# Kernel optimization log

Measured on AMD Instinct MI355X. Metric: run time of the kernel, lower is better.

Reference implementation:

```python
import jax, jax.numpy as jnp
import numpy as np

D_IN = 512
D = 1024      # new_embed_dim
H = 16        # num_heads
HD = D // H   # head_dim


def setup_inputs() -> dict:
    key = jax.random.key(0)
    ks = jax.random.split(key, 16)
    g = lambda k, shape, fan: jax.random.normal(k, shape, jnp.float32) / np.sqrt(fan)
    return {
        "x1": jax.random.normal(ks[0], (16, 1, D_IN), jnp.float32),
        "x2": jax.random.normal(ks[1], (16, 4096, D_IN), jnp.float32),
        "x3": jax.random.normal(ks[2], (16, 4096, D_IN), jnp.float32),
        # embedding1 (for x1) and embedding2 (used for BOTH x2 and x3, per source)
        "We1": g(ks[3], (D_IN, D), D_IN), "be1": jnp.zeros((D,), jnp.float32),
        "We2": g(ks[4], (D_IN, D), D_IN), "be2": jnp.zeros((D,), jnp.float32),
        "Wq": g(ks[5], (D, D), D), "bq": jnp.zeros((D,), jnp.float32),
        "Wk": g(ks[6], (D, D), D), "bk": jnp.zeros((D,), jnp.float32),
        "Wv": g(ks[7], (D, D), D), "bv": jnp.zeros((D,), jnp.float32),
        "Wo": g(ks[8], (D, D), D), "bo": jnp.zeros((D,), jnp.float32),
    }


def reference(x1, x2, x3, We1, be1, We2, be2, Wq, bq, Wk, bk, Wv, bv, Wo, bo):
    B = x1.shape[0]
    # embeddings (x3 intentionally uses embedding2's weights, matching source)
    x1e = x1 @ We1 + be1                      # [B,1,D]
    x2e = x2 @ We2 + be2                      # [B,S,D]
    x3e = x3 @ We2 + be2                      # [B,S,D]
    q = (x1e @ Wq + bq).reshape(B, -1, H, HD).transpose(0, 2, 1, 3)  # [B,H,1,HD]
    k = (x2e @ Wk + bk).reshape(B, -1, H, HD).transpose(0, 2, 1, 3)  # [B,H,S,HD]
    v = (x3e @ Wv + bv).reshape(B, -1, H, HD).transpose(0, 2, 1, 3)  # [B,H,S,HD]
    scale = jnp.asarray(np.sqrt(HD), q.dtype)
    attn = jax.nn.softmax(jnp.einsum("bhqd,bhkd->bhqk", q, k) / scale, axis=-1)
    # dropout is identity at inference (keras training=False default)
    av = jnp.einsum("bhqk,bhkd->bhqd", attn, v)          # [B,H,1,HD]
    av = av.transpose(0, 2, 1, 3).reshape(B, -1, D)      # [B,1,D]
    out = av @ Wo + bo                                   # [B,1,D]
    return jnp.squeeze(out, axis=1)                      # [B,D]
```

## Files before the change

kernel.cpp:

```cpp
#include <hip/hip_runtime.h>


#define DIN 512
#define DD  1024
#define NH  16
#define HD  64
#define BB  16
#define SS  4096
#define NCH 32

__device__ __forceinline__ int wave_id() {
    return __builtin_amdgcn_readfirstlane((int)(threadIdx.x >> 6));
}

__device__ __forceinline__ void tile_transpose(const float* __restrict__ in,
                                               float* __restrict__ out,
                                               int R, int C, int rblk, int cblk) {
    __shared__ float tl[32][33];
    const int tx = threadIdx.x & 31, ty = threadIdx.x >> 5;
    const int c0 = cblk * 32, r0 = rblk * 32;
#pragma unroll
    for (int k = 0; k < 4; ++k)
        tl[ty + k * 8][tx] = in[(size_t)(r0 + ty + k * 8) * C + c0 + tx];
    __syncthreads();
#pragma unroll
    for (int k = 0; k < 4; ++k)
        out[(size_t)(c0 + ty + k * 8) * R + r0 + tx] = tl[tx][ty + k * 8];
}

__global__ __launch_bounds__(256) void k_prep(const float* __restrict__ We2,
                                              const float* __restrict__ Wk,
                                              const float* __restrict__ be1,
                                              const float* __restrict__ bq,
                                              const float* __restrict__ bv,
                                              const float* __restrict__ bo,
                                              float* __restrict__ We2t,
                                              float* __restrict__ WkT,
                                              float* __restrict__ x1e,
                                              float* __restrict__ qb,
                                              float* __restrict__ av,
                                              float* __restrict__ out) {
    const int bx = blockIdx.x;
    if (bx < 512) {
        tile_transpose(We2, We2t, DIN, DD, bx >> 5, bx & 31);
    } else if (bx < 1536) {
        const int lb = bx - 512;
        tile_transpose(Wk, WkT, DD, DD, lb >> 5, lb & 31);
    } else {
        const int b = bx - 1536;
#pragma unroll
        for (int k = 0; k < 4; ++k) {
            const int c = k * 256 + threadIdx.x;
            x1e[(size_t)b * DD + c] = be1[c];
            qb[(size_t)b * DD + c]  = bq[c];
            av[(size_t)b * DD + c]  = bv[c];
            out[(size_t)b * DD + c] = bo[c];
        }
    }
}

template <int K, int N, int KS, bool HASB>
__global__ __launch_bounds__(256) void k_bmv2(const float* __restrict__ in,
                                              const float* __restrict__ W,
                                              const float* __restrict__ bias,
                                              float* __restrict__ out) {
    const int l = threadIdx.x & 63;
    const int c = blockIdx.x * 64 + l;
    const int wv = wave_id();
    constexpr int KCH = K / KS;
    constexpr int SUB = KCH / 4;
    const float* inb = in + (size_t)blockIdx.y * 16 * K;
    float acc[16];
#pragma unroll
    for (int r = 0; r < 16; ++r) acc[r] = 0.f;
    const int i0 = blockIdx.z * KCH + wv * SUB;
#pragma unroll 4
    for (int i = i0; i < i0 + SUB; ++i) {
        const float wval = W[(size_t)i * N + c];
#pragma unroll
        for (int r = 0; r < 16; ++r) acc[r] += inb[(size_t)r * K + i] * wval;
    }
    __shared__ float red[4][16][64];
#pragma unroll
    for (int r = 0; r < 16; ++r) red[wv][r][l] = acc[r];
    __syncthreads();
#pragma unroll
    for (int k = 0; k < 4; ++k) {
        const int r = wv + k * 4;
        float v = red[0][r][l] + red[1][r][l] + red[2][r][l] + red[3][r][l];
        float* dst = out + ((size_t)blockIdx.y * 16 + r) * N + c;
        if (KS == 1) {
            if (HASB) v += bias[c];
            *dst = v;
        } else {
            atomicAdd(dst, v);
        }
    }
}

__global__ __launch_bounds__(256) void k_u2(const float* __restrict__ q,
                                            const float* __restrict__ WkT,
                                            float* __restrict__ u) {
    const int h = blockIdx.y;
    const int l = threadIdx.x & 63;
    const int c = blockIdx.x * 64 + l;
    const int wv = wave_id();
    float acc[16];
#pragma unroll
    for (int bb = 0; bb < 16; ++bb) acc[bb] = 0.f;
#pragma unroll 4
    for (int dk = 0; dk < 16; ++dk) {
        const int d = wv * 16 + dk;
        const float wval = WkT[(size_t)(h * HD + d) * DD + c];
#pragma unroll
        for (int bb = 0; bb < 16; ++bb)
            acc[bb] += q[(size_t)bb * DD + h * HD + d] * wval;
    }
    __shared__ float red[4][16][64];
#pragma unroll
    for (int bb = 0; bb < 16; ++bb) red[wv][bb][l] = acc[bb];
    __syncthreads();
#pragma unroll
    for (int k = 0; k < 4; ++k) {
        const int bb = wv + k * 4;
        float v = red[0][bb][l] + red[1][bb][l] + red[2][bb][l] + red[3][bb][l];
        u[((size_t)bb * NH + h) * DD + c] = v;
    }
}

__global__ __launch_bounds__(256) void k_attn(const float* __restrict__ x2,
                                              const float* __restrict__ x3,
                                              const float* __restrict__ w,
                                              float* __restrict__ gp,
                                              float* __restrict__ mls) {
    __shared__ __align__(16) char smem[64 * 33 * 16 + 16 * 64 * 4];
    float4* tile = (float4*)smem;
    float*  scb  = (float*)(smem + 64 * 33 * 16);
    float*  red  = (float*)smem;
    __shared__ float sm[4][16], sl[4][16];

    const int b = blockIdx.y, ch = blockIdx.x;
    const int l = threadIdx.x & 63;
    const int wv = wave_id();
    const int h0 = wv * 4;
    const float4* wp = (const float4*)(w + ((size_t)b * NH + h0) * DIN);

    float m[16], lsum[16], acc[16][8];
#pragma unroll
    for (int h = 0; h < 16; ++h) {
        m[h] = -1e30f; lsum[h] = 0.f;
#pragma unroll
        for (int j = 0; j < 8; ++j) acc[h][j] = 0.f;
    }

    for (int t = 0; t < 2; ++t) {
        const int s0 = ch * 128 + t * 64;
        const float4* x2f = (const float4*)x2 + ((size_t)b * SS + s0) * (DIN / 4);
        float a0 = 0.f, a1 = 0.f, a2 = 0.f, a3 = 0.f;
        for (int kt = 0; kt < 4; ++kt) {
            __syncthreads();
#pragma unroll
            for (int k = 0; k < 8; ++k) {
                const int idx = threadIdx.x + k * 256;
                const int row = idx >> 5, c4 = idx & 31;
                tile[row * 33 + c4] = x2f[row * (DIN / 4) + kt * 32 + c4];
            }
            __syncthreads();
#pragma unroll 8
            for (int c4 = 0; c4 < 32; ++c4) {
                const float4 x = tile[l * 33 + c4];
                const float4 q0 = wp[kt * 32 + c4];
                const float4 q1 = wp[128 + kt * 32 + c4];
                const float4 q2 = wp[256 + kt * 32 + c4];
                const float4 q3 = wp[384 + kt * 32 + c4];
                a0 += x.x * q0.x + x.y * q0.y + x.z * q0.z + x.w * q0.w;
                a1 += x.x * q1.x + x.y * q1.y + x.z * q1.z + x.w * q1.w;
                a2 += x.x * q2.x + x.y * q2.y + x.z * q2.z + x.w * q2.w;
                a3 += x.x * q3.x + x.y * q3.y + x.z * q3.z + x.w * q3.w;
            }
        }
        scb[(h0 + 0) * 64 + l] = a0;
        scb[(h0 + 1) * 64 + l] = a1;
        scb[(h0 + 2) * 64 + l] = a2;
        scb[(h0 + 3) * 64 + l] = a3;
        __syncthreads();

        const int sq = wv * 16;
        float tm[16];
#pragma unroll
        for (int h = 0; h < 16; ++h) {
            float mm = -1e30f;
#pragma unroll
            for (int j = 0; j < 16; ++j) mm = fmaxf(mm, scb[h * 64 + sq + j]);
            tm[h] = mm * 0.125f;
        }
#pragma unroll
        for (int h = 0; h < 16; ++h) {
            const float mn = fmaxf(m[h], tm[h]);
            const float f = __expf(m[h] - mn);
            m[h] = mn; lsum[h] *= f;
#pragma unroll
            for (int j = 0; j < 8; ++j) acc[h][j] *= f;
        }
        for (int j = 0; j < 16; ++j) {
            const int s = s0 + sq + j;
            const float4* xr = (const float4*)(x3 + ((size_t)b * SS + s) * DIN);
            const float4 xa = xr[l];
            const float4 xb = xr[l + 64];
            const float xv[8] = {xa.x, xa.y, xa.z, xa.w, xb.x, xb.y, xb.z, xb.w};
#pragma unroll
            for (int h = 0; h < 16; ++h) {
                const float e = __expf(scb[h * 64 + sq + j] * 0.125f - m[h]);
                lsum[h] += e;
#pragma unroll
                for (int jj = 0; jj < 8; ++jj) acc[h][jj] += e * xv[jj];
            }
        }
    }

#pragma unroll
    for (int h = 0; h < 16; ++h) sm[wv][h] = m[h];
    __syncthreads();
#pragma unroll
    for (int h = 0; h < 16; ++h) {
        const float bmh = fmaxf(fmaxf(sm[0][h], sm[1][h]), fmaxf(sm[2][h], sm[3][h]));
        const float f = __expf(m[h] - bmh);
        lsum[h] *= f;
#pragma unroll
        for (int j = 0; j < 8; ++j) acc[h][j] *= f;
    }
#pragma unroll
    for (int h = 0; h < 16; ++h) sl[wv][h] = lsum[h];

#pragma unroll
    for (int hg = 0; hg < 4; ++hg) {
        __syncthreads();
#pragma unroll
        for (int hh = 0; hh < 4; ++hh) {
            const int hs = hg * 4 + hh;
            float* dst = &red[wv * 2048 + hh * 512];
            *(float4*)(dst + l * 4) =
                make_float4(acc[hs][0], acc[hs][1], acc[hs][2], acc[hs][3]);
            *(float4*)(dst + 256 + l * 4) =
                make_float4(acc[hs][4], acc[hs][5], acc[hs][6], acc[hs][7]);
        }
        __syncthreads();
        const int idx = threadIdx.x * 8;
        const int hh = idx >> 9;
        const int i = idx & 511;
        float o[8];
#pragma unroll
        for (int j = 0; j < 8; ++j)
            o[j] = red[0 * 2048 + idx + j] + red[1 * 2048 + idx + j] +
                   red[2 * 2048 + idx + j] + red[3 * 2048 + idx + j];
        float* dstg = gp + (((size_t)(b * NCH + ch) * NH) + hg * 4 + hh) * DIN + i;
        *(float4*)dstg = make_float4(o[0], o[1], o[2], o[3]);
        *(float4*)(dstg + 4) = make_float4(o[4], o[5], o[6], o[7]);
    }
    if (threadIdx.x < 16) {
        const int h = threadIdx.x;
        const float bmh = fmaxf(fmaxf(sm[0][h], sm[1][h]), fmaxf(sm[2][h], sm[3][h]));
        const float L = sl[0][h] + sl[1][h] + sl[2][h] + sl[3][h];
        float* dst = mls + (((size_t)b * NCH + ch) * NH + h) * 2;
        dst[0] = bmh;
        dst[1] = L;
    }
}

__global__ __launch_bounds__(256) void k_greduce2(const float* __restrict__ gp,
                                                  const float* __restrict__ mls,
                                                  float* __restrict__ g) {
    const int pair = blockIdx.x;
    const int b = pair >> 4, h = pair & 15;
    float M = -1e30f;
    for (int ch = 0; ch < NCH; ++ch)
        M = fmaxf(M, mls[(((size_t)b * NCH + ch) * NH + h) * 2]);
    float fch[NCH];
    float L = 0.f;
    for (int ch = 0; ch < NCH; ++ch) {
        const float* p = mls + (((size_t)b * NCH + ch) * NH + h) * 2;
        const float f = __expf(p[0] - M);
        fch[ch] = f;
        L += f * p[1];
    }
    const float invL = 1.f / L;
#pragma unroll
    for (int kk = 0; kk < 2; ++kk) {
        const int i = kk * 256 + threadIdx.x;
        float acc = 0.f;
        for (int ch = 0; ch < NCH; ++ch)
            acc += fch[ch] * gp[((size_t)(b * NCH + ch) * NH + h) * DIN + i];
        g[(size_t)pair * DIN + i] = acc * invL;
    }
}

__global__ __launch_bounds__(256) void k_av_at(const float* __restrict__ G2,
                                               const float* __restrict__ Wv,
                                               float* __restrict__ av) {
    const int h = blockIdx.x;
    const int l = threadIdx.x & 63;
    const int wv = wave_id();
    const int c0 = blockIdx.y * 128 + wv * 32;
    float acc[16];
#pragma unroll
    for (int bb = 0; bb < 16; ++bb) acc[bb] = 0.f;
#pragma unroll 4
    for (int c = c0; c < c0 + 32; ++c) {
        const float wval = Wv[(size_t)c * DD + h * HD + l];
#pragma unroll
        for (int bb = 0; bb < 16; ++bb)
            acc[bb] += G2[((size_t)bb * NH + h) * DD + c] * wval;
    }
    __shared__ float red[4][16][64];
#pragma unroll
    for (int bb = 0; bb < 16; ++bb) red[wv][bb][l] = acc[bb];
    __syncthreads();
#pragma unroll
    for (int k = 0; k < 4; ++k) {
        const int bb = wv + k * 4;
        float v = red[0][bb][l] + red[1][bb][l] + red[2][bb][l] + red[3][bb][l];
        atomicAdd(&av[(size_t)bb * DD + h * HD + l], v);
    }
}

extern "C" void kernel_launch(void* const* d_in, const int* in_sizes, int n_in,
                              void* d_out, int out_size, void* d_ws, size_t ws_size,
                              hipStream_t stream) {
    const float* x1  = (const float*)d_in[0];
    const float* x2  = (const float*)d_in[1];
    const float* x3  = (const float*)d_in[2];
    const float* We1 = (const float*)d_in[3];
    const float* be1 = (const float*)d_in[4];
    const float* We2 = (const float*)d_in[5];
    const float* be2 = (const float*)d_in[6];
    const float* Wq  = (const float*)d_in[7];
    const float* bq  = (const float*)d_in[8];
    const float* Wk  = (const float*)d_in[9];
    const float* bk  = (const float*)d_in[10];
    const float* Wv  = (const float*)d_in[11];
    const float* bv  = (const float*)d_in[12];
    const float* Wo  = (const float*)d_in[13];
    const float* bo  = (const float*)d_in[14];
    (void)bk;
    float* out = (float*)d_out;

    char* ws = (char*)d_ws;
    size_t off = 0;
    auto alloc = [&](size_t bytes) -> void* {
        void* p = ws + off;
        off = (off + bytes + 255) & ~(size_t)255;
        return p;
    };
    float* We2t = (float*)alloc((size_t)DD * DIN * 4);
    float* WkT  = (float*)alloc((size_t)DD * DD * 4);
    float* x1e  = (float*)alloc((size_t)BB * DD * 4);
    float* qb   = (float*)alloc((size_t)BB * DD * 4);
    float* u    = (float*)alloc((size_t)BB * NH * DD * 4);
    float* wv_  = (float*)alloc((size_t)BB * NH * DIN * 4);
    float* g    = (float*)alloc((size_t)BB * NH * DIN * 4);
    float* G2   = (float*)alloc((size_t)BB * NH * DD * 4);
    float* av   = (float*)alloc((size_t)BB * DD * 4);
    float* gp   = (float*)alloc((size_t)BB * NCH * NH * DIN * 4);
    float* mls  = (float*)alloc((size_t)BB * NCH * NH * 2 * 4);

    k_prep<<<1552, 256, 0, stream>>>(We2, Wk, be1, bq, bv, bo,
                                     We2t, WkT, x1e, qb, av, out);
    k_bmv2<DIN, DD, 8, false><<<dim3(DD / 64, 1, 8), 256, 0, stream>>>(x1, We1, nullptr, x1e);
    k_bmv2<DD, DD, 8, false><<<dim3(DD / 64, 1, 8), 256, 0, stream>>>(x1e, Wq, nullptr, qb);
    k_u2<<<dim3(DD / 64, NH), 256, 0, stream>>>(qb, WkT, u);
    k_bmv2<DD, DIN, 1, false><<<dim3(DIN / 64, BB * NH / 16, 1), 256, 0, stream>>>(u, We2t, nullptr, wv_);
    k_attn<<<dim3(NCH, BB), 256, 0, stream>>>(x2, x3, wv_, gp, mls);
    k_greduce2<<<BB * NH, 256, 0, stream>>>(gp, mls, g);
    k_bmv2<DIN, DD, 1, true><<<dim3(DD / 64, BB * NH / 16, 1), 256, 0, stream>>>(g, We2, be2, G2);
    k_av_at<<<dim3(NH, 8), 256, 0, stream>>>(G2, Wv, av);
    k_bmv2<DD, DD, 8, false><<<dim3(DD / 64, 1, 8), 256, 0, stream>>>(av, Wo, nullptr, out);
}
```

Measured before the change: 447.0 us.

## Split attention into 64-row chunks with per-wave head ownership and prefetch

```diff
diff --git a/kernel.cpp b/kernel.cpp
--- a/kernel.cpp
+++ b/kernel.cpp
@@ -7,7 +7,7 @@
 #define HD  64
 #define BB  16
 #define SS  4096
-#define NCH 32
+#define NCH 64
 
 __device__ __forceinline__ int wave_id() {
     return __builtin_amdgcn_readfirstlane((int)(threadIdx.x >> 6));
@@ -128,170 +128,129 @@
     }
 }
 
-__global__ __launch_bounds__(256) void k_attn(const float* __restrict__ x2,
-                                              const float* __restrict__ x3,
-                                              const float* __restrict__ w,
-                                              float* __restrict__ gp,
-                                              float* __restrict__ mls) {
-    __shared__ __align__(16) char smem[64 * 33 * 16 + 16 * 64 * 4];
-    float4* tile = (float4*)smem;
-    float*  scb  = (float*)(smem + 64 * 33 * 16);
-    float*  red  = (float*)smem;
-    __shared__ float sm[4][16], sl[4][16];
+__global__ __launch_bounds__(256, 4) void k_attn(const float* __restrict__ x2,
+                                                 const float* __restrict__ x3,
+                                                 const float* __restrict__ w,
+                                                 float* __restrict__ gp,
+                                                 float* __restrict__ mls) {
+    __shared__ __align__(16) float4 tile[64 * 33];
+    float* etab = (float*)tile;
 
     const int b = blockIdx.y, ch = blockIdx.x;
     const int l = threadIdx.x & 63;
     const int wv = wave_id();
     const int h0 = wv * 4;
+    const int s0 = ch * 64;
     const float4* wp = (const float4*)(w + ((size_t)b * NH + h0) * DIN);
-
-    float m[16], lsum[16], acc[16][8];
-#pragma unroll
-    for (int h = 0; h < 16; ++h) {
-        m[h] = -1e30f; lsum[h] = 0.f;
-#pragma unroll
-        for (int j = 0; j < 8; ++j) acc[h][j] = 0.f;
-    }
-
-    for (int t = 0; t < 2; ++t) {
-        const int s0 = ch * 128 + t * 64;
-        const float4* x2f = (const float4*)x2 + ((size_t)b * SS + s0) * (DIN / 4);
-        float a0 = 0.f, a1 = 0.f, a2 = 0.f, a3 = 0.f;
-        for (int kt = 0; kt < 4; ++kt) {
-            __syncthreads();
-#pragma unroll
-            for (int k = 0; k < 8; ++k) {
-                const int idx = threadIdx.x + k * 256;
-                const int row = idx >> 5, c4 = idx & 31;
-                tile[row * 33 + c4] = x2f[row * (DIN / 4) + kt * 32 + c4];
-            }
-            __syncthreads();
+    const float4* x2f = (const float4*)x2 + ((size_t)b * SS + s0) * (DIN / 4);
+
+    float a0 = 0.f, a1 = 0.f, a2 = 0.f, a3 = 0.f;
+    for (int kt = 0; kt < 4; ++kt) {
+#pragma unroll
+        for (int k = 0; k < 8; ++k) {
+            const int idx = threadIdx.x + k * 256;
+            const int row = idx >> 5, c4 = idx & 31;
+            tile[row * 33 + c4] = x2f[(size_t)row * 128 + kt * 32 + c4];
+        }
+        __syncthreads();
 #pragma unroll 8
-            for (int c4 = 0; c4 < 32; ++c4) {
-                const float4 x = tile[l * 33 + c4];
-                const float4 q0 = wp[kt * 32 + c4];
-                const float4 q1 = wp[128 + kt * 32 + c4];
-                const float4 q2 = wp[256 + kt * 32 + c4];
-                const float4 q3 = wp[384 + kt * 32 + c4];
-                a0 += x.x * q0.x + x.y * q0.y + x.z * q0.z + x.w * q0.w;
-                a1 += x.x * q1.x + x.y * q1.y + x.z * q1.z + x.w * q1.w;
-                a2 += x.x * q2.x + x.y * q2.y + x.z * q2.z + x.w * q2.w;
-                a3 += x.x * q3.x + x.y * q3.y + x.z * q3.z + x.w * q3.w;
-            }
-        }
-        scb[(h0 + 0) * 64 + l] = a0;
-        scb[(h0 + 1) * 64 + l] = a1;
-        scb[(h0 + 2) * 64 + l] = a2;
-        scb[(h0 + 3) * 64 + l] = a3;
+        for (int c4 = 0; c4 < 32; ++c4) {
+            const float4 x = tile[l * 33 + c4];
+            const float4 q0 = wp[kt * 32 + c4];
+            const float4 q1 = wp[128 + kt * 32 + c4];
+            const float4 q2 = wp[256 + kt * 32 + c4];
+            const float4 q3 = wp[384 + kt * 32 + c4];
+            a0 += x.x * q0.x + x.y * q0.y + x.z * q0.z + x.w * q0.w;
+            a1 += x.x * q1.x + x.y * q1.y + x.z * q1.z + x.w * q1.w;
+            a2 += x.x * q2.x + x.y * q2.y + x.z * q2.z + x.w * q2.w;
+            a3 += x.x * q3.x + x.y * q3.y + x.z * q3.z + x.w * q3.w;
+        }
         __syncthreads();
-
-        const int sq = wv * 16;
-        float tm[16];
-#pragma unroll
-        for (int h = 0; h < 16; ++h) {
-            float mm = -1e30f;
-#pragma unroll
-            for (int j = 0; j < 16; ++j) mm = fmaxf(mm, scb[h * 64 + sq + j]);
-            tm[h] = mm * 0.125f;
-        }
-#pragma unroll
-        for (int h = 0; h < 16; ++h) {
-            const float mn = fmaxf(m[h], tm[h]);
-            const float f = __expf(m[h] - mn);
-            m[h] = mn; lsum[h] *= f;
-#pragma unroll
-            for (int j = 0; j < 8; ++j) acc[h][j] *= f;
-        }
-        for (int j = 0; j < 16; ++j) {
-            const int s = s0 + sq + j;
-            const float4* xr = (const float4*)(x3 + ((size_t)b * SS + s) * DIN);
-            const float4 xa = xr[l];
-            const float4 xb = xr[l + 64];
-            const float xv[8] = {xa.x, xa.y, xa.z, xa.w, xb.x, xb.y, xb.z, xb.w};
-#pragma unroll
-            for (int h = 0; h < 16; ++h) {
-                const float e = __expf(scb[h * 64 + sq + j] * 0.125f - m[h]);
-                lsum[h] += e;
-#pragma unroll
-                for (int jj = 0; jj < 8; ++jj) acc[h][jj] += e * xv[jj];
-            }
-        }
-    }
-
-#pragma unroll
-    for (int h = 0; h < 16; ++h) sm[wv][h] = m[h];
-    __syncthreads();
-#pragma unroll
-    for (int h = 0; h < 16; ++h) {
-        const float bmh = fmaxf(fmaxf(sm[0][h], sm[1][h]), fmaxf(sm[2][h], sm[3][h]));
-        const float f = __expf(m[h] - bmh);
-        lsum[h] *= f;
-#pragma unroll
-        for (int j = 0; j < 8; ++j) acc[h][j] *= f;
-    }
-#pragma unroll
-    for (int h = 0; h < 16; ++h) sl[wv][h] = lsum[h];
-
-#pragma unroll
-    for (int hg = 0; hg < 4; ++hg) {
-        __syncthreads();
-#pragma unroll
-        for (int hh = 0; hh < 4; ++hh) {
-            const int hs = hg * 4 + hh;
-            float* dst = &red[wv * 2048 + hh * 512];
-            *(float4*)(dst + l * 4) =
-                make_float4(acc[hs][0], acc[hs][1], acc[hs][2], acc[hs][3]);
-            *(float4*)(dst + 256 + l * 4) =
-                make_float4(acc[hs][4], acc[hs][5], acc[hs][6], acc[hs][7]);
-        }
-        __syncthreads();
-        const int idx = threadIdx.x * 8;
-        const int hh = idx >> 9;
-        const int i = idx & 511;
-        float o[8];
-#pragma unroll
-        for (int j = 0; j < 8; ++j)
-            o[j] = red[0 * 2048 + idx + j] + red[1 * 2048 + idx + j] +
-                   red[2 * 2048 + idx + j] + red[3 * 2048 + idx + j];
-        float* dstg = gp + (((size_t)(b * NCH + ch) * NH) + hg * 4 + hh) * DIN + i;
-        *(float4*)dstg = make_float4(o[0], o[1], o[2], o[3]);
-        *(float4*)(dstg + 4) = make_float4(o[4], o[5], o[6], o[7]);
-    }
-    if (threadIdx.x < 16) {
-        const int h = threadIdx.x;
-        const float bmh = fmaxf(fmaxf(sm[0][h], sm[1][h]), fmaxf(sm[2][h], sm[3][h]));
-        const float L = sl[0][h] + sl[1][h] + sl[2][h] + sl[3][h];
-        float* dst = mls + (((size_t)b * NCH + ch) * NH + h) * 2;
-        dst[0] = bmh;
-        dst[1] = L;
+    }
+
+    const float sc0 = a0 * 0.125f, sc1 = a1 * 0.125f;
+    const float sc2 = a2 * 0.125f, sc3 = a3 * 0.125f;
+    float mh[4] = {sc0, sc1, sc2, sc3};
+#pragma unroll
+    for (int k = 0; k < 4; ++k) {
+#pragma unroll
+        for (int off = 1; off < 64; off <<= 1)
+            mh[k] = fmaxf(mh[k], __shfl_xor(mh[k], off));
+    }
+
+    const float4 ev = make_float4(__expf(sc0 - mh[0]), __expf(sc1 - mh[1]),
+                                  __expf(sc2 - mh[2]), __expf(sc3 - mh[3]));
+    *(float4*)&etab[(wv * 64 + l) * 4] = ev;
+
+    const float4* xr = (const float4*)(x3 + ((size_t)b * SS + s0) * DIN);
+    float acc[4][8];
+#pragma unroll
+    for (int k = 0; k < 4; ++k)
+#pragma unroll
+        for (int jj = 0; jj < 8; ++jj) acc[k][jj] = 0.f;
+    float ls[4] = {0.f, 0.f, 0.f, 0.f};
+
+    float4 pa = xr[l], pb = xr[64 + l];
+    float4 na = xr[128 + l], nb = xr[192 + l];
+#pragma unroll 4
+    for (int j = 0; j < 64; ++j) {
+        const float4 xa = pa, xb = pb;
+        pa = na; pb = nb;
+        const int jn = (j + 2 < 64) ? (j + 2) : 63;
+        na = xr[(size_t)jn * 128 + l];
+        nb = xr[(size_t)jn * 128 + 64 + l];
+        const float4 e4 = *(const float4*)&etab[(wv * 64 + j) * 4];
+        const float ee[4] = {e4.x, e4.y, e4.z, e4.w};
+        const float xv[8] = {xa.x, xa.y, xa.z, xa.w, xb.x, xb.y, xb.z, xb.w};
+#pragma unroll
+        for (int k = 0; k < 4; ++k) {
+            ls[k] += ee[k];
+#pragma unroll
+            for (int jj = 0; jj < 8; ++jj) acc[k][jj] += ee[k] * xv[jj];
+        }
+    }
+
+    float* gb = gp + ((size_t)(b * NCH + ch) * NH + h0) * DIN;
+#pragma unroll
+    for (int k = 0; k < 4; ++k) {
+        *(float4*)(gb + (size_t)k * DIN + 4 * l) =
+            make_float4(acc[k][0], acc[k][1], acc[k][2], acc[k][3]);
+        *(float4*)(gb + (size_t)k * DIN + 256 + 4 * l) =
+            make_float4(acc[k][4], acc[k][5], acc[k][6], acc[k][7]);
+    }
+    if (l == 0) {
+#pragma unroll
+        for (int k = 0; k < 4; ++k) {
+            float* dst = mls + (((size_t)b * NCH + ch) * NH + h0 + k) * 2;
+            dst[0] = mh[k];
+            dst[1] = ls[k];
+        }
     }
 }
 
 __global__ __launch_bounds__(256) void k_greduce2(const float* __restrict__ gp,
                                                   const float* __restrict__ mls,
                                                   float* __restrict__ g) {
-    const int pair = blockIdx.x;
+    const int bx = blockIdx.x;
+    const int pair = bx >> 1;
     const int b = pair >> 4, h = pair & 15;
+    const int i = (bx & 1) * 256 + threadIdx.x;
+    const float* mbase = mls + ((size_t)b * NCH * NH + h) * 2;
     float M = -1e30f;
+#pragma unroll 8
     for (int ch = 0; ch < NCH; ++ch)
-        M = fmaxf(M, mls[(((size_t)b * NCH + ch) * NH + h) * 2]);
-    float fch[NCH];
+        M = fmaxf(M, mbase[(size_t)ch * NH * 2]);
     float L = 0.f;
-    for (int ch = 0; ch < NCH; ++ch) {
-        const float* p = mls + (((size_t)b * NCH + ch) * NH + h) * 2;
-        const float f = __expf(p[0] - M);
-        fch[ch] = f;
-        L += f * p[1];
-    }
+#pragma unroll 8
+    for (int ch = 0; ch < NCH; ++ch)
+        L += __expf(mbase[(size_t)ch * NH * 2] - M) * mbase[(size_t)ch * NH * 2 + 1];
     const float invL = 1.f / L;
-#pragma unroll
-    for (int kk = 0; kk < 2; ++kk) {
-        const int i = kk * 256 + threadIdx.x;
-        float acc = 0.f;
-        for (int ch = 0; ch < NCH; ++ch)
-            acc += fch[ch] * gp[((size_t)(b * NCH + ch) * NH + h) * DIN + i];
-        g[(size_t)pair * DIN + i] = acc * invL;
-    }
+    const float* gpb = gp + ((size_t)(b * NCH) * NH + h) * DIN + i;
+    float acc = 0.f;
+#pragma unroll 8
+    for (int ch = 0; ch < NCH; ++ch)
+        acc += __expf(mbase[(size_t)ch * NH * 2] - M) * gpb[(size_t)ch * NH * DIN];
+    g[(size_t)pair * DIN + i] = acc * invL;
 }
 
 __global__ __launch_bounds__(256) void k_av_at(const float* __restrict__ G2,
@@ -370,7 +329,7 @@
     k_u2<<<dim3(DD / 64, NH), 256, 0, stream>>>(qb, WkT, u);
     k_bmv2<DD, DIN, 1, false><<<dim3(DIN / 64, BB * NH / 16, 1), 256, 0, stream>>>(u, We2t, nullptr, wv_);
     k_attn<<<dim3(NCH, BB), 256, 0, stream>>>(x2, x3, wv_, gp, mls);
-    k_greduce2<<<BB * NH, 256, 0, stream>>>(gp, mls, g);
+    k_greduce2<<<BB * NH * 2, 256, 0, stream>>>(gp, mls, g);
     k_bmv2<DIN, DD, 1, true><<<dim3(DD / 64, BB * NH / 16, 1), 256, 0, stream>>>(g, We2, be2, G2);
     k_av_at<<<dim3(NH, 8), 256, 0, stream>>>(G2, Wv, av);
     k_bmv2<DD, DD, 8, false><<<dim3(DD / 64, 1, 8), 256, 0, stream>>>(av, Wo, nullptr, out);
```

After: 452.8 us. About the same (+1.3%).
